# Optimization experiments

Hardware: AMD Instinct MI355X
Metric: run time of the kernel (lower is better)

Reference implementation:

```python
import jax, jax.numpy as jnp
import numpy as np

HIDDEN = 2048
FFN = 2048      # ffn_hidden_size (tp_size == 1)
E = 8           # moe_num_experts
TOP_K = 2       # moe_top_k
S = 2048        # number of tokens


def setup_inputs() -> dict:
    key = jax.random.key(0)
    k1, k2, k3, k4 = jax.random.split(key, 4)
    return {
        "hidden_states": jax.random.normal(k1, (S, HIDDEN), jnp.float32),
        "w_qkv": jax.random.normal(k2, (3 * E, HIDDEN), jnp.float32) * 0.02,
        "w1": jax.random.normal(k3, (E, HIDDEN, 2 * FFN), jnp.float32) * 0.02,
        "w2": jax.random.normal(k4, (E, FFN, HIDDEN), jnp.float32) * 0.02,
        "top_k": TOP_K,
    }


def reference(hidden_states, w_qkv, w1, w2, top_k):
    S, H = hidden_states.shape
    # --- ParallelAttention_router (gate), computed in fp32 as in the source ---
    mix = hidden_states @ w_qkv.T                                  # [S, 3E]
    q, k, v = jnp.split(mix.astype(jnp.float32), 3, axis=-1)       # each [S, E]
    # attn_weights[s,i,j] = q[s,i]*k[s,j]; softmax over j; logits = attn @ v
    attn = jax.nn.softmax(q[:, :, None] * k[:, None, :], axis=-1)  # [S, E, E]
    logits = jnp.einsum('sij,sj->si', attn, v)                     # [S, E]
    # --- top-k routing: softmax over selected logits ---
    top_logits, indices = jax.lax.top_k(logits, top_k)             # [S, K]
    scores = jax.nn.softmax(top_logits, axis=-1).astype(hidden_states.dtype)
    # --- experts: per-expert GLU MLP. The torch code sorts tokens by expert and
    # runs a grouped-GEMM loop; mathematically out[s] = sum_k scores[s,k] *
    # MLP_{indices[s,k]}(x[s]). We compute all experts densely (static shapes)
    # and gather/combine, which is the same math. ---
    fc1 = jnp.einsum('sh,ehi->esi', hidden_states, w1)             # [E, S, 2*FFN]
    g, u = jnp.split(fc1, 2, axis=-1)
    inter = jax.nn.silu(g) * u                                     # [E, S, FFN]
    expert_out = jnp.einsum('esi,eih->esh', inter, w2)             # [E, S, H]
    tok = jnp.arange(S)
    out = jnp.zeros_like(hidden_states)
    for kk in range(top_k):  # tiny static loop over top_k (=2)
        out = out + scores[:, kk, None] * expert_out[indices[:, kk], tok]
    return out
```

## Files before the change

### kernel.cpp

```cpp
#include <hip/hip_runtime.h>
#include <math.h>

#define S_TOK 2048
#define HID   2048
#define FFN_  2048
#define NEXP  8
#define CAP   2048

typedef short  s8v __attribute__((ext_vector_type(8)));
typedef short  s4v __attribute__((ext_vector_type(4)));
typedef float  f4v __attribute__((ext_vector_type(4)));

__device__ __forceinline__ unsigned short f32_bf16(float f){
  unsigned u = __float_as_uint(f);
  u += 0x7fffu + ((u>>16)&1u);
  return (unsigned short)(u>>16);
}
__device__ __forceinline__ int lds_off(int r,int kq){
  return (r*4 + (kq ^ ((r>>2)&3)))*8;
}
__device__ __forceinline__ void gl_lds16(const unsigned short* g, unsigned short* l){
  __builtin_amdgcn_global_load_lds(
      (const __attribute__((address_space(1))) unsigned int*)(const void*)g,
      (__attribute__((address_space(3))) unsigned int*)(void*)l,
      16, 0, 0);
}

__global__ __launch_bounds__(256) void prep_k(
    const float* __restrict__ X,  unsigned short* __restrict__ Xb,
    const float* __restrict__ W1, unsigned short* __restrict__ W1t,
    const float* __restrict__ W2, unsigned short* __restrict__ W2t,
    float* __restrict__ out, int* __restrict__ hdr)
{
  const int bid = blockIdx.x, tid = threadIdx.x;
  __shared__ __align__(16) unsigned short t[128*66];

  if (bid < 4096){
    if (bid==0 && tid<8) hdr[tid] = 0;
    int i = (bid*256 + tid)*4;
    f4v z = {0.f,0.f,0.f,0.f};
    *reinterpret_cast<f4v*>(out + i) = z;
    return;
  }
  if (bid < 6144){
    int i = ((bid-4096)*256 + tid)*8;
    f4v a = *reinterpret_cast<const f4v*>(X + i);
    f4v b = *reinterpret_cast<const f4v*>(X + i + 4);
    s8v o;
    o[0]=(short)f32_bf16(a[0]); o[1]=(short)f32_bf16(a[1]);
    o[2]=(short)f32_bf16(a[2]); o[3]=(short)f32_bf16(a[3]);
    o[4]=(short)f32_bf16(b[0]); o[5]=(short)f32_bf16(b[1]);
    o[6]=(short)f32_bf16(b[2]); o[7]=(short)f32_bf16(b[3]);
    *reinterpret_cast<s8v*>(Xb + i) = o;
    return;
  }
  const float* src; unsigned short* dst; int K,N,n0,k0,e;
  if (bid < 14336){
    int b = bid - 6144; e = b>>10; int rem = b&1023;
    N = 4096; K = 2048; n0 = (rem&31)*128; k0 = (rem>>5)*64;
    src = W1; dst = W1t;
  } else {
    int b = bid - 14336; e = b>>9; int rem = b&511;
    N = 2048; K = 2048; n0 = (rem&15)*128; k0 = (rem>>4)*64;
    src = W2; dst = W2t;
  }
  src += (size_t)e*K*N + (size_t)k0*N + n0;
  dst += (size_t)e*N*K + (size_t)n0*K + k0;
  const int nb = tid & 31;
  const int kb = tid >> 5;
  f4v f[8];
  #pragma unroll
  for (int j=0;j<8;j++)
    f[j] = *reinterpret_cast<const f4v*>(src + (size_t)(kb*8+j)*N + nb*4);
  #pragma unroll
  for (int c=0;c<4;c++){
    int n = nb*4 + c;
    s8v v;
    #pragma unroll
    for (int j=0;j<8;j++) v[j] = (short)f32_bf16(f[j][c]);
    *reinterpret_cast<s8v*>(&t[n*66 + ((kb ^ ((n>>5)&3))*8)]) = v;
  }
  __syncthreads();
  #pragma unroll
  for (int p=0;p<4;p++){
    int n = p*32 + (tid>>3);
    int c = tid & 7;
    s8v v = *reinterpret_cast<const s8v*>(&t[n*66 + ((c ^ ((n>>5)&3))*8)]);
    *reinterpret_cast<s8v*>(dst + (size_t)n*K + c*8) = v;
  }
}

__global__ __launch_bounds__(64) void router_k(
    const float* __restrict__ X, const float* __restrict__ Wqkv,
    int* __restrict__ hdr, int* __restrict__ tok_slot, float* __restrict__ scr_slot)
{
  const int s = blockIdx.x, lane = threadIdx.x;
  const float* x = X + (size_t)s*HID;
  f4v xv[8];
  #pragma unroll
  for (int i=0;i<8;i++) xv[i] = *reinterpret_cast<const f4v*>(x + (i*64+lane)*4);
  float dot[24];
  #pragma unroll
  for (int o=0;o<24;o++){
    const float* w = Wqkv + (size_t)o*HID;
    float a = 0.f;
    #pragma unroll
    for (int i=0;i<8;i++){
      f4v wv = *reinterpret_cast<const f4v*>(w + (i*64+lane)*4);
      a += xv[i][0]*wv[0] + xv[i][1]*wv[1] + xv[i][2]*wv[2] + xv[i][3]*wv[3];
    }
    #pragma unroll
    for (int off=32; off; off>>=1) a += __shfl_xor(a, off, 64);
    dot[o] = a;
  }
  if (lane==0){
    float lg[8];
    #pragma unroll
    for (int i=0;i<8;i++){
      float qi = dot[i];
      float mx = -1e30f;
      #pragma unroll
      for (int j=0;j<8;j++) mx = fmaxf(mx, qi*dot[8+j]);
      float se=0.f, lv=0.f;
      #pragma unroll
      for (int j=0;j<8;j++){
        float e = expf(qi*dot[8+j] - mx);
        se += e; lv += e*dot[16+j];
      }
      lg[i] = lv/se;
    }
    int i0=0; float v0=lg[0];
    #pragma unroll
    for (int i=1;i<8;i++) if (lg[i]>v0){v0=lg[i];i0=i;}
    int i1=-1; float v1=-1e30f;
    #pragma unroll
    for (int i=0;i<8;i++) if (i!=i0 && lg[i]>v1){v1=lg[i];i1=i;}
    float a  = expf(v1-v0);
    float s0 = 1.f/(1.f+a);
    int p0 = atomicAdd(&hdr[i0],1);
    int p1 = atomicAdd(&hdr[i1],1);
    tok_slot[i0*CAP+p0] = s;  scr_slot[i0*CAP+p0] = s0;
    tok_slot[i1*CAP+p1] = s;  scr_slot[i1*CAP+p1] = a*s0;
  }
}

__global__ __launch_bounds__(256,3) void gemm1_k(
    const unsigned short* __restrict__ Xb, const unsigned short* __restrict__ W1t,
    const int* __restrict__ hdr, const int* __restrict__ tok_slot,
    unsigned short* __restrict__ inter)
{
  const int bid = blockIdx.x;
  const int swz = (bid&7)*512 + (bid>>3);
  const int e = swz>>9, rem = swz&511, nt = rem>>4, mt = rem&15;
  const int cnt = hdr[e];
  const int m0  = mt*128;
  if (m0 >= cnt) return;
  const int off = e*CAP;
  const int n0  = nt*64;
  const unsigned short* W1e = W1t + (size_t)e*(2*FFN_)*HID;

  __shared__ __align__(16) unsigned short sA[128*32];
  __shared__ __align__(16) unsigned short sB[128*32];
  __shared__ int sTok[128];

  const int tid = threadIdx.x;
  if (tid < 128){
    int r = m0 + tid; if (r >= cnt) r = cnt-1;
    sTok[tid] = tok_slot[off + r];
  }
  __syncthreads();

  const int lane = tid & 63, wv = tid >> 6;
  const int wm = wv >> 1, wn = wv & 1;
  const int lm = lane & 15, kq = lane >> 4;
  const int srow = lane >> 2, kg = lane & 3;
  const int kgs  = kg ^ ((srow >> 2)&3);

  const unsigned short* gA0 = Xb + (size_t)sTok[wv*16 + srow]*HID      + kgs*8;
  const unsigned short* gA1 = Xb + (size_t)sTok[64 + wv*16 + srow]*HID + kgs*8;
  const unsigned short* gB0 = W1e + (size_t)(n0 + wv*16 + srow)*HID        + kgs*8;
  const unsigned short* gB1 = W1e + (size_t)(FFN_ + n0 + wv*16 + srow)*HID + kgs*8;
  unsigned short* lA0 = sA + (wv*16)*32;
  unsigned short* lA1 = sA + (64 + wv*16)*32;
  unsigned short* lB0 = sB + (wv*16)*32;
  unsigned short* lB1 = sB + (64 + wv*16)*32;

  f4v zero = {0.f,0.f,0.f,0.f};
  f4v acc[2][2][4];
  #pragma unroll
  for (int a=0;a<2;a++)
    #pragma unroll
    for (int b=0;b<2;b++)
      #pragma unroll
      for (int c=0;c<4;c++) acc[a][b][c]=zero;

  for (int k0=0; k0<HID; k0+=32){
    gl_lds16(gA0, lA0); gl_lds16(gA1, lA1);
    gl_lds16(gB0, lB0); gl_lds16(gB1, lB1);
    gA0 += 32; gA1 += 32; gB0 += 32; gB1 += 32;
    __syncthreads();
    s8v af[4], bfr[2][2];
    #pragma unroll
    for (int mf=0;mf<4;mf++)
      af[mf] = *reinterpret_cast<const s8v*>(&sA[lds_off(wm*64+mf*16+lm, kq)]);
    #pragma unroll
    for (int st=0; st<2; st++)
      #pragma unroll
      for (int nf=0;nf<2;nf++)
        bfr[st][nf] = *reinterpret_cast<const s8v*>(&sB[lds_off(st*64+wn*32+nf*16+lm, kq)]);
    #pragma unroll
    for (int st=0; st<2; st++)
      #pragma unroll
      for (int nf=0;nf<2;nf++)
        #pragma unroll
        for (int mf=0;mf<4;mf++)
          acc[st][nf][mf] = __builtin_amdgcn_mfma_f32_16x16x32_bf16(
              af[mf], bfr[st][nf], acc[st][nf][mf], 0,0,0);
    __syncthreads();
  }
  const int lq = lane>>4;
  #pragma unroll
  for (int nf=0;nf<2;nf++)
    #pragma unroll
    for (int mf=0;mf<4;mf++){
      f4v g = acc[0][nf][mf], u = acc[1][nf][mf];
      #pragma unroll
      for (int r=0;r<4;r++){
        int row = wm*64 + mf*16 + lq*4 + r;
        if (m0+row < cnt){
          float gv = g[r];
          float val = gv / (1.f + expf(-gv)) * u[r];
          inter[(size_t)(off+m0+row)*FFN_ + n0 + wn*32 + nf*16 + lm] = f32_bf16(val);
        }
      }
    }
}

__global__ __launch_bounds__(256,3) void gemm2_k(
    const unsigned short* __restrict__ inter, const unsigned short* __restrict__ W2t,
    const int* __restrict__ hdr, const int* __restrict__ tok_slot,
    const float* __restrict__ scr_slot, float* __restrict__ out)
{
  const int bid = blockIdx.x;
  const int swz = (bid&7)*256 + (bid>>3);
  const int e = swz>>8, rem = swz&255, nt = rem>>4, mt = rem&15;
  const int cnt = hdr[e];
  const int m0  = mt*128;
  if (m0 >= cnt) return;
  const int off = e*CAP;
  const int n0  = nt*128;
  const unsigned short* W2e = W2t + (size_t)e*HID*FFN_;

  __shared__ __align__(16) unsigned short sA[128*32];
  __shared__ __align__(16) unsigned short sB[128*32];
  __shared__ int   sTok[128];
  __shared__ float sScr[128];

  const int tid = threadIdx.x;
  if (tid < 128){
    int r = m0 + tid; if (r >= cnt) r = cnt-1;
    sTok[tid] = tok_slot[off + r];
    sScr[tid] = scr_slot[off + r];
  }

  const int lane = tid & 63, wv = tid >> 6;
  const int wm = wv >> 1, wn = wv & 1;
  const int lm = lane & 15, kq = lane >> 4;
  const int srow = lane >> 2, kg = lane & 3;
  const int kgs  = kg ^ ((srow >> 2)&3);

  int r0 = m0 + wv*16 + srow;      if (r0 >= cnt) r0 = cnt-1;
  int r1 = m0 + 64 + wv*16 + srow; if (r1 >= cnt) r1 = cnt-1;
  const unsigned short* gA0 = inter + (size_t)(off + r0)*FFN_ + kgs*8;
  const unsigned short* gA1 = inter + (size_t)(off + r1)*FFN_ + kgs*8;
  const unsigned short* gB0 = W2e + (size_t)(n0 + wv*16 + srow)*FFN_      + kgs*8;
  const unsigned short* gB1 = W2e + (size_t)(n0 + 64 + wv*16 + srow)*FFN_ + kgs*8;
  unsigned short* lA0 = sA + (wv*16)*32;
  unsigned short* lA1 = sA + (64 + wv*16)*32;
  unsigned short* lB0 = sB + (wv*16)*32;
  unsigned short* lB1 = sB + (64 + wv*16)*32;

  f4v zero = {0.f,0.f,0.f,0.f};
  f4v acc[4][4];
  #pragma unroll
  for (int a=0;a<4;a++)
    #pragma unroll
    for (int b=0;b<4;b++) acc[a][b]=zero;

  __syncthreads();

  for (int k0=0; k0<FFN_; k0+=32){
    gl_lds16(gA0, lA0); gl_lds16(gA1, lA1);
    gl_lds16(gB0, lB0); gl_lds16(gB1, lB1);
    gA0 += 32; gA1 += 32; gB0 += 32; gB1 += 32;
    __syncthreads();
    s8v af[4], bfr[4];
    #pragma unroll
    for (int mf=0;mf<4;mf++)
      af[mf] = *reinterpret_cast<const s8v*>(&sA[lds_off(wm*64+mf*16+lm, kq)]);
    #pragma unroll
    for (int nf=0;nf<4;nf++)
      bfr[nf] = *reinterpret_cast<const s8v*>(&sB[lds_off(wn*64+nf*16+lm, kq)]);
    #pragma unroll
    for (int nf=0;nf<4;nf++)
      #pragma unroll
      for (int mf=0;mf<4;mf++)
        acc[nf][mf] = __builtin_amdgcn_mfma_f32_16x16x32_bf16(
            af[mf], bfr[nf], acc[nf][mf], 0,0,0);
    __syncthreads();
  }
  const int lq = lane>>4;
  #pragma unroll
  for (int nf=0;nf<4;nf++)
    #pragma unroll
    for (int mf=0;mf<4;mf++)
      #pragma unroll
      for (int r=0;r<4;r++){
        int row = wm*64 + mf*16 + lq*4 + r;
        if (m0+row < cnt)
          atomicAdd(&out[(size_t)sTok[row]*HID + n0 + wn*64 + nf*16 + lm],
                    acc[nf][mf][r]*sScr[row]);
      }
}

extern "C" void kernel_launch(void* const* d_in, const int* in_sizes, int n_in,
                              void* d_out, int out_size, void* d_ws, size_t ws_size,
                              hipStream_t stream)
{
  const float* X    = (const float*)d_in[0];
  const float* Wqkv = (const float*)d_in[1];
  const float* W1   = (const float*)d_in[2];
  const float* W2   = (const float*)d_in[3];
  float* out = (float*)d_out;

  char* ws = (char*)d_ws;
  int*   hdr      = (int*)ws;
  int*   tok_slot = (int*)(ws + 4096);
  float* scr_slot = (float*)(ws + 4096 + 65536);
  size_t o = 4096 + 2*65536;
  unsigned short* Xb    = (unsigned short*)(ws + o); o += (size_t)S_TOK*HID*2;
  unsigned short* inter = (unsigned short*)(ws + o); o += (size_t)NEXP*CAP*FFN_*2;
  unsigned short* W1t   = (unsigned short*)(ws + o); o += (size_t)NEXP*2*FFN_*HID*2;
  unsigned short* W2t   = (unsigned short*)(ws + o);

  prep_k   <<<18432, 256, 0, stream>>>(X, Xb, W1, W1t, W2, W2t, out, hdr);
  router_k <<<S_TOK, 64,  0, stream>>>(X, Wqkv, hdr, tok_slot, scr_slot);
  gemm1_k  <<<4096,  256, 0, stream>>>(Xb, W1t, hdr, tok_slot, inter);
  gemm2_k  <<<2048,  256, 0, stream>>>(inter, W2t, hdr, tok_slot, scr_slot, out);
}
```

Baseline: 777.4 us.

## Fuse router into prep kernel and enlarge weight-transpose tiles

Moves the router computation into the prep kernel as extra blocks (4 tokens per 256-thread block), so the separate router launch disappears and routing overlaps with the weight conversion. The bf16 transpose of W1/W2 now uses 64x256 tiles, with 16 rows per thread and a wider swizzled LDS buffer, giving fewer and larger blocks. Zeroing and X conversion now handle 16 elements per thread, and the header reset moves to a hipMemsetAsync call. The larger tiles use more LDS and registers per block, which may lower occupancy.

Measured after the change: 777.3 us. Within noise of the previous version (-0.0%).

```diff
diff --git a/kernel.cpp b/kernel.cpp
--- a/kernel.cpp
+++ b/kernel.cpp
@@ -30,117 +30,135 @@
     const float* __restrict__ X,  unsigned short* __restrict__ Xb,
     const float* __restrict__ W1, unsigned short* __restrict__ W1t,
     const float* __restrict__ W2, unsigned short* __restrict__ W2t,
-    float* __restrict__ out, int* __restrict__ hdr)
+    const float* __restrict__ Wqkv,
+    float* __restrict__ out, int* __restrict__ hdr,
+    int* __restrict__ tok_slot, float* __restrict__ scr_slot)
 {
   const int bid = blockIdx.x, tid = threadIdx.x;
-  __shared__ __align__(16) unsigned short t[128*66];
-
-  if (bid < 4096){
-    if (bid==0 && tid<8) hdr[tid] = 0;
-    int i = (bid*256 + tid)*4;
+  __shared__ __align__(16) unsigned short t[64*264];
+
+  if (bid < 512){
+    const int lane = tid & 63;
+    const int s = bid*4 + (tid >> 6);
+    const float* x = X + (size_t)s*HID;
+    f4v xv[8];
+    #pragma unroll
+    for (int i=0;i<8;i++) xv[i] = *reinterpret_cast<const f4v*>(x + (i*64+lane)*4);
+    float dot[24];
+    #pragma unroll
+    for (int o=0;o<24;o++){
+      const float* w = Wqkv + (size_t)o*HID;
+      float a = 0.f;
+      #pragma unroll
+      for (int i=0;i<8;i++){
+        f4v wv = *reinterpret_cast<const f4v*>(w + (i*64+lane)*4);
+        a += xv[i][0]*wv[0] + xv[i][1]*wv[1] + xv[i][2]*wv[2] + xv[i][3]*wv[3];
+      }
+      #pragma unroll
+      for (int off=32; off; off>>=1) a += __shfl_xor(a, off, 64);
+      dot[o] = a;
+    }
+    if (lane==0){
+      float lg[8];
+      #pragma unroll
+      for (int i=0;i<8;i++){
+        float qi = dot[i];
+        float mx = -1e30f;
+        #pragma unroll
+        for (int j=0;j<8;j++) mx = fmaxf(mx, qi*dot[8+j]);
+        float se=0.f, lv=0.f;
+        #pragma unroll
+        for (int j=0;j<8;j++){
+          float e = expf(qi*dot[8+j] - mx);
+          se += e; lv += e*dot[16+j];
+        }
+        lg[i] = lv/se;
+      }
+      int i0=0; float v0=lg[0];
+      #pragma unroll
+      for (int i=1;i<8;i++) if (lg[i]>v0){v0=lg[i];i0=i;}
+      int i1=-1; float v1=-1e30f;
+      #pragma unroll
+      for (int i=0;i<8;i++) if (i!=i0 && lg[i]>v1){v1=lg[i];i1=i;}
+      float a  = expf(v1-v0);
+      float s0 = 1.f/(1.f+a);
+      int p0 = atomicAdd(&hdr[i0],1);
+      int p1 = atomicAdd(&hdr[i1],1);
+      tok_slot[i0*CAP+p0] = s;  scr_slot[i0*CAP+p0] = s0;
+      tok_slot[i1*CAP+p1] = s;  scr_slot[i1*CAP+p1] = a*s0;
+    }
+    return;
+  }
+  if (bid < 6656){
+    const float* src; unsigned short* dst; int N, n0, k0;
+    if (bid < 4608){
+      int b = bid - 512; int e = b>>9; int rem = b&511;
+      N = 4096; n0 = (rem&63)*64; k0 = (rem>>6)*256;
+      src = W1 + (size_t)e*2048*4096; dst = W1t + (size_t)e*4096*2048;
+    } else {
+      int b = bid - 4608; int e = b>>8; int rem = b&255;
+      N = 2048; n0 = (rem&31)*64; k0 = (rem>>5)*256;
+      src = W2 + (size_t)e*2048*2048; dst = W2t + (size_t)e*2048*2048;
+    }
+    src += (size_t)k0*N + n0;
+    dst += (size_t)n0*2048 + k0;
+    const int nb = tid & 15;
+    const int kb = tid >> 4;
+    s8v col[4][2];
+    #pragma unroll
+    for (int j=0;j<16;j++){
+      f4v f = *reinterpret_cast<const f4v*>(src + (size_t)(kb*16+j)*N + nb*4);
+      #pragma unroll
+      for (int c=0;c<4;c++)
+        ((unsigned short*)&col[c][j>>3])[j&7] = f32_bf16(f[c]);
+    }
+    #pragma unroll
+    for (int c=0;c<4;c++){
+      int n = nb*4 + c;
+      #pragma unroll
+      for (int h=0;h<2;h++){
+        int g  = kb*2 + h;
+        int gs = g ^ (nb & 7);
+        *reinterpret_cast<s8v*>(&t[n*264 + gs*8]) = col[c][h];
+      }
+    }
+    __syncthreads();
+    #pragma unroll
+    for (int p=0;p<8;p++){
+      int idx = p*256 + tid;
+      int n = idx >> 5, g = idx & 31;
+      int gs = g ^ ((n>>2) & 7);
+      s8v v = *reinterpret_cast<const s8v*>(&t[n*264 + gs*8]);
+      *reinterpret_cast<s8v*>(dst + (size_t)n*2048 + g*8) = v;
+    }
+    return;
+  }
+  if (bid < 7680){
+    int i = ((bid-6656)*256 + tid)*16;
     f4v z = {0.f,0.f,0.f,0.f};
-    *reinterpret_cast<f4v*>(out + i) = z;
+    *reinterpret_cast<f4v*>(out + i)      = z;
+    *reinterpret_cast<f4v*>(out + i + 4)  = z;
+    *reinterpret_cast<f4v*>(out + i + 8)  = z;
+    *reinterpret_cast<f4v*>(out + i + 12) = z;
     return;
   }
-  if (bid < 6144){
-    int i = ((bid-4096)*256 + tid)*8;
+  {
+    int i = ((bid-7680)*256 + tid)*16;
     f4v a = *reinterpret_cast<const f4v*>(X + i);
     f4v b = *reinterpret_cast<const f4v*>(X + i + 4);
-    s8v o;
-    o[0]=(short)f32_bf16(a[0]); o[1]=(short)f32_bf16(a[1]);
-    o[2]=(short)f32_bf16(a[2]); o[3]=(short)f32_bf16(a[3]);
-    o[4]=(short)f32_bf16(b[0]); o[5]=(short)f32_bf16(b[1]);
-    o[6]=(short)f32_bf16(b[2]); o[7]=(short)f32_bf16(b[3]);
-    *reinterpret_cast<s8v*>(Xb + i) = o;
-    return;
-  }
-  const float* src; unsigned short* dst; int K,N,n0,k0,e;
-  if (bid < 14336){
-    int b = bid - 6144; e = b>>10; int rem = b&1023;
-    N = 4096; K = 2048; n0 = (rem&31)*128; k0 = (rem>>5)*64;
-    src = W1; dst = W1t;
-  } else {
-    int b = bid - 14336; e = b>>9; int rem = b&511;
-    N = 2048; K = 2048; n0 = (rem&15)*128; k0 = (rem>>4)*64;
-    src = W2; dst = W2t;
-  }
-  src += (size_t)e*K*N + (size_t)k0*N + n0;
-  dst += (size_t)e*N*K + (size_t)n0*K + k0;
-  const int nb = tid & 31;
-  const int kb = tid >> 5;
-  f4v f[8];
-  #pragma unroll
-  for (int j=0;j<8;j++)
-    f[j] = *reinterpret_cast<const f4v*>(src + (size_t)(kb*8+j)*N + nb*4);
-  #pragma unroll
-  for (int c=0;c<4;c++){
-    int n = nb*4 + c;
-    s8v v;
-    #pragma unroll
-    for (int j=0;j<8;j++) v[j] = (short)f32_bf16(f[j][c]);
-    *reinterpret_cast<s8v*>(&t[n*66 + ((kb ^ ((n>>5)&3))*8)]) = v;
-  }
-  __syncthreads();
-  #pragma unroll
-  for (int p=0;p<4;p++){
-    int n = p*32 + (tid>>3);
-    int c = tid & 7;
-    s8v v = *reinterpret_cast<const s8v*>(&t[n*66 + ((c ^ ((n>>5)&3))*8)]);
-    *reinterpret_cast<s8v*>(dst + (size_t)n*K + c*8) = v;
-  }
-}
-
-__global__ __launch_bounds__(64) void router_k(
-    const float* __restrict__ X, const float* __restrict__ Wqkv,
-    int* __restrict__ hdr, int* __restrict__ tok_slot, float* __restrict__ scr_slot)
-{
-  const int s = blockIdx.x, lane = threadIdx.x;
-  const float* x = X + (size_t)s*HID;
-  f4v xv[8];
-  #pragma unroll
-  for (int i=0;i<8;i++) xv[i] = *reinterpret_cast<const f4v*>(x + (i*64+lane)*4);
-  float dot[24];
-  #pragma unroll
-  for (int o=0;o<24;o++){
-    const float* w = Wqkv + (size_t)o*HID;
-    float a = 0.f;
-    #pragma unroll
-    for (int i=0;i<8;i++){
-      f4v wv = *reinterpret_cast<const f4v*>(w + (i*64+lane)*4);
-      a += xv[i][0]*wv[0] + xv[i][1]*wv[1] + xv[i][2]*wv[2] + xv[i][3]*wv[3];
-    }
-    #pragma unroll
-    for (int off=32; off; off>>=1) a += __shfl_xor(a, off, 64);
-    dot[o] = a;
-  }
-  if (lane==0){
-    float lg[8];
-    #pragma unroll
-    for (int i=0;i<8;i++){
-      float qi = dot[i];
-      float mx = -1e30f;
-      #pragma unroll
-      for (int j=0;j<8;j++) mx = fmaxf(mx, qi*dot[8+j]);
-      float se=0.f, lv=0.f;
-      #pragma unroll
-      for (int j=0;j<8;j++){
-        float e = expf(qi*dot[8+j] - mx);
-        se += e; lv += e*dot[16+j];
-      }
-      lg[i] = lv/se;
-    }
-    int i0=0; float v0=lg[0];
-    #pragma unroll
-    for (int i=1;i<8;i++) if (lg[i]>v0){v0=lg[i];i0=i;}
-    int i1=-1; float v1=-1e30f;
-    #pragma unroll
-    for (int i=0;i<8;i++) if (i!=i0 && lg[i]>v1){v1=lg[i];i1=i;}
-    float a  = expf(v1-v0);
-    float s0 = 1.f/(1.f+a);
-    int p0 = atomicAdd(&hdr[i0],1);
-    int p1 = atomicAdd(&hdr[i1],1);
-    tok_slot[i0*CAP+p0] = s;  scr_slot[i0*CAP+p0] = s0;
-    tok_slot[i1*CAP+p1] = s;  scr_slot[i1*CAP+p1] = a*s0;
+    f4v c = *reinterpret_cast<const f4v*>(X + i + 8);
+    f4v d = *reinterpret_cast<const f4v*>(X + i + 12);
+    s8v o0, o1;
+    o0[0]=(short)f32_bf16(a[0]); o0[1]=(short)f32_bf16(a[1]);
+    o0[2]=(short)f32_bf16(a[2]); o0[3]=(short)f32_bf16(a[3]);
+    o0[4]=(short)f32_bf16(b[0]); o0[5]=(short)f32_bf16(b[1]);
+    o0[6]=(short)f32_bf16(b[2]); o0[7]=(short)f32_bf16(b[3]);
+    o1[0]=(short)f32_bf16(c[0]); o1[1]=(short)f32_bf16(c[1]);
+    o1[2]=(short)f32_bf16(c[2]); o1[3]=(short)f32_bf16(c[3]);
+    o1[4]=(short)f32_bf16(d[0]); o1[5]=(short)f32_bf16(d[1]);
+    o1[6]=(short)f32_bf16(d[2]); o1[7]=(short)f32_bf16(d[3]);
+    *reinterpret_cast<s8v*>(Xb + i)     = o0;
+    *reinterpret_cast<s8v*>(Xb + i + 8) = o1;
   }
 }
 
@@ -343,8 +361,9 @@
   unsigned short* W1t   = (unsigned short*)(ws + o); o += (size_t)NEXP*2*FFN_*HID*2;
   unsigned short* W2t   = (unsigned short*)(ws + o);
 
-  prep_k   <<<18432, 256, 0, stream>>>(X, Xb, W1, W1t, W2, W2t, out, hdr);
-  router_k <<<S_TOK, 64,  0, stream>>>(X, Wqkv, hdr, tok_slot, scr_slot);
+  hipMemsetAsync(hdr, 0, 32, stream);
+  prep_k   <<<8704,  256, 0, stream>>>(X, Xb, W1, W1t, W2, W2t, Wqkv, out, hdr,
+                                       tok_slot, scr_slot);
   gemm1_k  <<<4096,  256, 0, stream>>>(Xb, W1t, hdr, tok_slot, inter);
   gemm2_k  <<<2048,  256, 0, stream>>>(inter, W2t, hdr, tok_slot, scr_slot, out);
 }
```
